# Optimization experiments

Hardware: AMD Instinct MI355X
Metric: run time of the kernel (lower is better)

Reference implementation:

```python
import jax, jax.numpy as jnp
import numpy as np

N, M, T = 8, 4, 500000   # state dim, measurement dim, trajectory length
ITERS = 100


def setup_inputs() -> dict:
    key = jax.random.key(0)
    k1, k2, k3, k4 = jax.random.split(key, 4)
    xs = jax.random.normal(k1, (N, T), dtype=jnp.float32)
    ys = jax.random.normal(k2, (M, T), dtype=jnp.float32)
    # Well-conditioned, stable models: F near identity, modest H, SPD noise covs.
    F = jnp.eye(N, dtype=jnp.float32) + 0.01 * jax.random.normal(k3, (N, N), dtype=jnp.float32)
    H = 0.1 * jax.random.normal(k4, (M, N), dtype=jnp.float32)
    Q = jnp.eye(N, dtype=jnp.float32)
    R = jnp.eye(M, dtype=jnp.float32)
    gamma = jnp.float32(0.01)
    return {"xs": xs, "ys": ys, "F": F, "H": H, "Q": Q, "R": R, "gamma": gamma}


def reference(xs, ys, F, H, Q, R, gamma):
    # Precompute the message operators (done once in __init__ in the original).
    Qinv = jnp.linalg.inv(Q)
    Rinv = jnp.linalg.inv(R)
    negQinv = -Qinv            # n x n
    FtQinv = F.T @ Qinv        # n x n
    HtRinv = H.T @ Rinv        # n x m

    def step(x, _):
        # x: n x T. Shift columns to get x_{t-1} and x_{t+1} (edge-replicated).
        x_past = jnp.concatenate([x[:, :1], x[:, :-1]], axis=1)
        x_fut = jnp.concatenate([x[:, 1:], x[:, -1:]], axis=1)
        # diff_past_curr: x_t - F x_{t-1}, with ROW 0 zeroed (faithful to res[0]=0.0)
        d1 = (x - F @ x_past).at[0].set(0.0)
        # diff_curr_fut: x_{t+1} - F x_t, with LAST ROW zeroed (faithful to res[-1]=0.0)
        d2 = (x_fut - F @ x).at[-1].set(0.0)
        # diff_y_curr: y - H x_t
        d3 = ys - H @ x
        m = negQinv @ d1 + FtQinv @ d2 + HtRinv @ d3
        return x + gamma * m, None

    x, _ = jax.lax.scan(step, xs, None, length=ITERS)
    return x
```

## Files before the change

kernel.cpp:

```cpp
#include <hip/hip_runtime.h>

#define TLEN   500000
#define NITER  100
#define DHALF  6
#define NOFF   (2*DHALF+1)
#define STRIP  20
#define EWIN   32
#define CT     256
#define NCONV  ((TLEN - 2*STRIP + CT - 1) / CT)

__global__ __launch_bounds__(256) void band_and_edges(
    const float* __restrict__ xs, const float* __restrict__ ys,
    const float* __restrict__ F, const float* __restrict__ H,
    const float* __restrict__ Q, const float* __restrict__ R,
    const float* __restrict__ gam,
    float* __restrict__ wout,
    float* __restrict__ out)
{
  __shared__ double dQaug[8][16];
  __shared__ double dRaug[4][8];
  __shared__ double dFtQi[64], dHtRi[32], dA1[64], dB2[64];
  __shared__ float fmats[224];
  __shared__ __align__(16) float st[2][34][8];

  const int tid = threadIdx.x;
  const int b   = blockIdx.x;
  const int r8  = (tid >> 3) & 7;
  const int c8  = tid & 7;

  if (tid < 64) {
    dQaug[r8][c8]     = (double)Q[r8*8 + c8];
    dQaug[r8][c8 + 8] = (c8 == r8) ? 1.0 : 0.0;
  } else if (tid < 96) {
    int t = tid - 64, rr = t >> 3, cr = t & 7;
    dRaug[rr][cr] = (cr < 4) ? (double)R[rr*4 + cr] : ((cr - 4 == rr) ? 1.0 : 0.0);
  }
  __syncthreads();
  for (int col = 0; col < 8; ++col) {
    double piv = 1, fq = 0, p1 = 0, p2 = 0, m1 = 0, m2 = 0;
    double rpiv = 1, frr = 0, pr = 0, mr = 0;
    const bool doQ = tid < 64;
    const bool doR = (tid >= 64 && tid < 96 && col < 4);
    if (doQ) {
      piv = dQaug[col][col]; fq = dQaug[r8][col];
      p1 = dQaug[col][c8];   p2 = dQaug[col][c8 + 8];
      m1 = dQaug[r8][c8];    m2 = dQaug[r8][c8 + 8];
    }
    if (doR) {
      int t = tid - 64, rr = t >> 3, cr = t & 7;
      rpiv = dRaug[col][col]; frr = dRaug[rr][col];
      pr = dRaug[col][cr];    mr = dRaug[rr][cr];
    }
    __syncthreads();
    if (doQ) {
      dQaug[r8][c8]     = (r8 == col) ? m1 / piv : m1 - fq * (p1 / piv);
      dQaug[r8][c8 + 8] = (r8 == col) ? m2 / piv : m2 - fq * (p2 / piv);
    }
    if (doR) {
      int t = tid - 64, rr = t >> 3, cr = t & 7;
      dRaug[rr][cr] = (rr == col) ? mr / rpiv : mr - frr * (pr / rpiv);
    }
    __syncthreads();
  }
  if (tid < 64) {
    double s = 0.0;
    #pragma unroll
    for (int k = 0; k < 8; ++k) s += (double)F[k*8 + r8] * dQaug[k][c8 + 8];
    dFtQi[r8*8 + c8] = s;
    dA1[r8*8 + c8] = (c8 == 0) ? 0.0 : -dQaug[r8][c8 + 8];
  } else if (tid < 96) {
    int t = tid - 64, i = t >> 2, j = t & 3;
    double s = 0.0;
    #pragma unroll
    for (int k = 0; k < 4; ++k) s += (double)H[k*8 + i] * dRaug[k][j + 4];
    dHtRi[i*4 + j] = s;
  }
  __syncthreads();
  if (tid < 64) dB2[r8*8 + c8] = (c8 == 7) ? 0.0 : dFtQi[r8*8 + c8];
  __syncthreads();
  {
    const double g = (double)gam[0];
    if (tid < 64) {
      double sp = 0.0;
      #pragma unroll
      for (int k = 0; k < 8; ++k) sp -= dA1[r8*8 + k] * (double)F[k*8 + c8];
      double t2 = dA1[r8*8 + c8];
      #pragma unroll
      for (int k = 0; k < 8; ++k) t2 -= dB2[r8*8 + k] * (double)F[k*8 + c8];
      #pragma unroll
      for (int k = 0; k < 4; ++k) t2 -= dHtRi[r8*4 + k] * (double)H[k*8 + c8];
      fmats[       c8*8 + r8] = (float)(((r8 == c8) ? 1.0 : 0.0) + g * t2);
      fmats[ 64 +  c8*8 + r8] = (float)(g * sp);
      fmats[128 +  c8*8 + r8] = (float)(g * dB2[r8*8 + c8]);
    } else if (tid < 96) {
      int t = tid - 64, i = t >> 2, j = t & 3;
      fmats[192 + j*8 + i] = (float)(g * dHtRi[i*4 + j]);
    }
  }
  __syncthreads();

  const int i = tid & 7;
  const int g = tid >> 3;
  float cmr[8], pmr[8], fur[7];
  #pragma unroll
  for (int k = 0; k < 8; ++k) {
    cmr[k] = fmats[       k*8 + i];
    pmr[k] = fmats[ 64 +  k*8 + i];
    if (k < 7) fur[k] = fmats[128 + k*8 + i];
  }
  float* const stf = (float*)st;
  const int BUF = 34*8;

  if (b < 12) {
    const int c = b;
    const bool act = tid < NOFF*8;
    const int s = g + 1;
    for (int idx = tid; idx < 2*BUF; idx += 256) stf[idx] = 0.0f;
    __syncthreads();
    if (act && c < 8 && s == DHALF + 1 && i == c) st[0][s][i] = 1.0f;
    const float seed = (act && c >= 8 && s == DHALF + 1) ? fmats[192 + (c - 8)*8 + i] : 0.0f;
    __syncthreads();
    int p = 0;
    float last = 0.0f;
    #pragma unroll 1
    for (int it = 0; it < NITER; ++it) {
      if (act) {
        const float* sp_ = stf + p*BUF;
        const float4 o0 = *(const float4*)(sp_ + s*8);
        const float4 o1 = *(const float4*)(sp_ + s*8 + 4);
        const float4 u0 = *(const float4*)(sp_ + (s + 1)*8);
        const float4 u1 = *(const float4*)(sp_ + (s + 1)*8 + 4);
        const float4 d0 = *(const float4*)(sp_ + (s - 1)*8);
        const float4 d1 = *(const float4*)(sp_ + (s - 1)*8 + 4);
        float a0 = seed, a1 = 0.0f, a2 = 0.0f;
        a0 = fmaf(cmr[0], o0.x, a0); a0 = fmaf(cmr[1], o0.y, a0);
        a0 = fmaf(cmr[2], o0.z, a0); a0 = fmaf(cmr[3], o0.w, a0);
        a0 = fmaf(cmr[4], o1.x, a0); a0 = fmaf(cmr[5], o1.y, a0);
        a0 = fmaf(cmr[6], o1.z, a0); a0 = fmaf(cmr[7], o1.w, a0);
        a1 = fmaf(pmr[0], u0.x, a1); a1 = fmaf(pmr[1], u0.y, a1);
        a1 = fmaf(pmr[2], u0.z, a1); a1 = fmaf(pmr[3], u0.w, a1);
        a1 = fmaf(pmr[4], u1.x, a1); a1 = fmaf(pmr[5], u1.y, a1);
        a1 = fmaf(pmr[6], u1.z, a1); a1 = fmaf(pmr[7], u1.w, a1);
        a2 = fmaf(fur[0], d0.x, a2); a2 = fmaf(fur[1], d0.y, a2);
        a2 = fmaf(fur[2], d0.z, a2); a2 = fmaf(fur[3], d0.w, a2);
        a2 = fmaf(fur[4], d1.x, a2); a2 = fmaf(fur[5], d1.y, a2);
        a2 = fmaf(fur[6], d1.z, a2);
        last = a0 + a1 + a2;
        stf[(p^1)*BUF + s*8 + i] = last;
      }
      __syncthreads();
      p ^= 1;
    }
    if (act) wout[(c*NOFF + (s - 1))*8 + i] = last;
    return;
  }

  const bool left = (b == 12);
  const int col  = g;
  const int gcol = left ? col : (TLEN - EWIN + col);
  const int sL = (col > 0) ? col - 1 : 0;
  const int sR = (col < EWIN - 1) ? col + 1 : EWIN - 1;
  const float xv = xs[i*TLEN + gcol];
  float gyv;
  {
    gyv = fmats[192 +      i] * ys[0*TLEN + gcol];
    gyv = fmaf(fmats[192 +  8 + i], ys[1*TLEN + gcol], gyv);
    gyv = fmaf(fmats[192 + 16 + i], ys[2*TLEN + gcol], gyv);
    gyv = fmaf(fmats[192 + 24 + i], ys[3*TLEN + gcol], gyv);
  }
  st[0][col][i] = xv;
  __syncthreads();
  int p = 0;
  float last = xv;
  #pragma unroll 1
  for (int it = 0; it < NITER; ++it) {
    const float* sp_ = stf + p*BUF;
    const float4 o0 = *(const float4*)(sp_ + col*8);
    const float4 o1 = *(const float4*)(sp_ + col*8 + 4);
    const float4 l0 = *(const float4*)(sp_ + sL*8);
    const float4 l1 = *(const float4*)(sp_ + sL*8 + 4);
    const float4 q0 = *(const float4*)(sp_ + sR*8);
    const float4 q1 = *(const float4*)(sp_ + sR*8 + 4);
    float a0 = gyv, a1 = 0.0f, a2 = 0.0f;
    a0 = fmaf(cmr[0], o0.x, a0); a0 = fmaf(cmr[1], o0.y, a0);
    a0 = fmaf(cmr[2], o0.z, a0); a0 = fmaf(cmr[3], o0.w, a0);
    a0 = fmaf(cmr[4], o1.x, a0); a0 = fmaf(cmr[5], o1.y, a0);
    a0 = fmaf(cmr[6], o1.z, a0); a0 = fmaf(cmr[7], o1.w, a0);
    a1 = fmaf(pmr[0], l0.x, a1); a1 = fmaf(pmr[1], l0.y, a1);
    a1 = fmaf(pmr[2], l0.z, a1); a1 = fmaf(pmr[3], l0.w, a1);
    a1 = fmaf(pmr[4], l1.x, a1); a1 = fmaf(pmr[5], l1.y, a1);
    a1 = fmaf(pmr[6], l1.z, a1); a1 = fmaf(pmr[7], l1.w, a1);
    a2 = fmaf(fur[0], q0.x, a2); a2 = fmaf(fur[1], q0.y, a2);
    a2 = fmaf(fur[2], q0.z, a2); a2 = fmaf(fur[3], q0.w, a2);
    a2 = fmaf(fur[4], q1.x, a2); a2 = fmaf(fur[5], q1.y, a2);
    a2 = fmaf(fur[6], q1.z, a2);
    last = a0 + a1 + a2;
    stf[(p^1)*BUF + col*8 + i] = last;
    __syncthreads();
    p ^= 1;
  }
  if (left ? (col < STRIP) : (col >= EWIN - STRIP)) out[i*TLEN + gcol] = last;
}

__global__ __launch_bounds__(CT) void kgm_conv(
    const float* __restrict__ xs, const float* __restrict__ ys,
    const float* __restrict__ wq, float* __restrict__ out)
{
  const int tid  = threadIdx.x;
  const int ocol = STRIP + blockIdx.x * CT + tid;
  const int col  = (ocol < TLEN - STRIP) ? ocol : (TLEN - STRIP - 1);

  float acc[8] = {0,0,0,0,0,0,0,0};
  #pragma unroll
  for (int k = 0; k < 12; ++k) {
    const float* src = (k < 8) ? (xs + k*TLEN + col) : (ys + (k-8)*TLEN + col);
    const float* wk  = wq + k*(NOFF*8);
    float z[NOFF];
    #pragma unroll
    for (int d = 0; d < NOFF; ++d) z[d] = src[d - DHALF];
    #pragma unroll
    for (int d = 0; d < NOFF; ++d) {
      #pragma unroll
      for (int i = 0; i < 8; ++i)
        acc[i] = fmaf(wk[d*8 + i], z[d], acc[i]);
    }
  }

  if (ocol < TLEN - STRIP) {
    #pragma unroll
    for (int i = 0; i < 8; ++i) out[i*TLEN + ocol] = acc[i];
  }
}

extern "C" void kernel_launch(void* const* d_in, const int* in_sizes, int n_in,
                              void* d_out, int out_size, void* d_ws, size_t ws_size,
                              hipStream_t stream)
{
  (void)in_sizes; (void)n_in; (void)out_size; (void)ws_size;
  const float* xs = (const float*)d_in[0];
  const float* ys = (const float*)d_in[1];
  const float* F  = (const float*)d_in[2];
  const float* H  = (const float*)d_in[3];
  const float* Q  = (const float*)d_in[4];
  const float* R  = (const float*)d_in[5];
  const float* ga = (const float*)d_in[6];
  float* ws  = (float*)d_ws;
  float* out = (float*)d_out;
  band_and_edges<<<14, 256, 0, stream>>>(xs, ys, F, H, Q, R, ga, ws, out);
  kgm_conv<<<NCONV, CT, 0, stream>>>(xs, ys, ws, out);
}
```

Before: 53.23 us.

## Compute two columns per thread in conv kernel with LDS-staged weights

The banded convolution kernel now gives each thread two adjacent output columns. Each input row is read once as float2 loads over a 14-wide window and shared across both outputs, and the per-offset weights are staged into LDS with a padded 128-float row stride and read as float4. The weight workspace layout is changed to that padded stride, with the pad zero-filled by the band kernel. Block size drops to 64 threads and the grid halves. This is meant to cut redundant global loads and weight fetches per FMA, at the cost of more registers and fewer threads in flight.

```diff
diff --git a/kernel.cpp b/kernel.cpp
--- a/kernel.cpp
+++ b/kernel.cpp
@@ -6,8 +6,10 @@
 #define NOFF   (2*DHALF+1)
 #define STRIP  20
 #define EWIN   32
-#define CT     256
-#define NCONV  ((TLEN - 2*STRIP + CT - 1) / CT)
+#define CT     64
+#define CCPT   2
+#define NCONV  ((TLEN - 2*STRIP + CT*CCPT - 1) / (CT*CCPT))
+#define WROW   128
 
 __global__ __launch_bounds__(256) void band_and_edges(
     const float* __restrict__ xs, const float* __restrict__ ys,
@@ -151,7 +153,8 @@
       __syncthreads();
       p ^= 1;
     }
-    if (act) wout[(c*NOFF + (s - 1))*8 + i] = last;
+    if (act) wout[c*WROW + (s - 1)*8 + i] = last;
+    if (tid >= NOFF*8 && tid < WROW) wout[c*WROW + tid] = 0.0f;
     return;
   }
 
@@ -206,29 +209,53 @@
     const float* __restrict__ xs, const float* __restrict__ ys,
     const float* __restrict__ wq, float* __restrict__ out)
 {
-  const int tid  = threadIdx.x;
-  const int ocol = STRIP + blockIdx.x * CT + tid;
-  const int col  = (ocol < TLEN - STRIP) ? ocol : (TLEN - STRIP - 1);
-
-  float acc[8] = {0,0,0,0,0,0,0,0};
+  __shared__ __align__(16) float wl[12 * WROW];
+  const int lane = threadIdx.x;
   #pragma unroll
+  for (int t = 0; t < 6; ++t) {
+    const int idx = lane + t*64;
+    *(float4*)(wl + 4*idx) = *(const float4*)(wq + 4*idx);
+  }
+  __syncthreads();
+
+  const int ocol = STRIP + (blockIdx.x * CT + lane) * CCPT;
+  const int col0 = (ocol <= TLEN - STRIP - CCPT) ? ocol : (TLEN - STRIP - CCPT);
+
+  float2 acc[8];
+  #pragma unroll
+  for (int i = 0; i < 8; ++i) acc[i] = make_float2(0.f, 0.f);
+
+  #pragma unroll 2
   for (int k = 0; k < 12; ++k) {
-    const float* src = (k < 8) ? (xs + k*TLEN + col) : (ys + (k-8)*TLEN + col);
-    const float* wk  = wq + k*(NOFF*8);
-    float z[NOFF];
-    #pragma unroll
-    for (int d = 0; d < NOFF; ++d) z[d] = src[d - DHALF];
+    const float* src = ((k < 8) ? (xs + k*TLEN) : (ys + (k-8)*TLEN)) + col0;
+    float z[14];
+    #pragma unroll
+    for (int h = 0; h < 7; ++h) {
+      float2 v = *(const float2*)(src - 6 + 2*h);
+      z[2*h] = v.x; z[2*h + 1] = v.y;
+    }
+    const float* wk = wl + k*WROW;
     #pragma unroll
     for (int d = 0; d < NOFF; ++d) {
       #pragma unroll
-      for (int i = 0; i < 8; ++i)
-        acc[i] = fmaf(wk[d*8 + i], z[d], acc[i]);
+      for (int j = 0; j < 2; ++j) {
+        const float4 w4 = *(const float4*)(wk + d*8 + 4*j);
+        acc[4*j+0].x = fmaf(w4.x, z[d],     acc[4*j+0].x);
+        acc[4*j+0].y = fmaf(w4.x, z[d + 1], acc[4*j+0].y);
+        acc[4*j+1].x = fmaf(w4.y, z[d],     acc[4*j+1].x);
+        acc[4*j+1].y = fmaf(w4.y, z[d + 1], acc[4*j+1].y);
+        acc[4*j+2].x = fmaf(w4.z, z[d],     acc[4*j+2].x);
+        acc[4*j+2].y = fmaf(w4.z, z[d + 1], acc[4*j+2].y);
+        acc[4*j+3].x = fmaf(w4.w, z[d],     acc[4*j+3].x);
+        acc[4*j+3].y = fmaf(w4.w, z[d + 1], acc[4*j+3].y);
+      }
     }
   }
 
   if (ocol < TLEN - STRIP) {
     #pragma unroll
-    for (int i = 0; i < 8; ++i) out[i*TLEN + ocol] = acc[i];
+    for (int i = 0; i < 8; ++i)
+      *(float2*)(out + i*TLEN + ocol) = acc[i];
   }
 }
 
```

After: 52.06 us. 2.2% less time.

## Restructure band convolution to register-tile 8 columns per thread with split-K halves

Applied to the files above, without the earlier changes.

The convolution kernel now gives each thread 8 consecutive output columns for one output row, loading input strips with float4 reads and holding that row's weights in registers. The 12 input channels are split between two halves of the block, which are combined through shared memory. The band kernel also writes the weights in a transposed, padded layout to support this. The goal is to cut redundant global loads (previously 13 scalar loads per channel per column) and per-FMA weight loads, at the cost of more registers (80 weights plus 24 inputs), a shared-memory reduction, and a barrier.

```diff
diff --git a/kernel.cpp b/kernel.cpp
--- a/kernel.cpp
+++ b/kernel.cpp
@@ -6,8 +6,9 @@
 #define NOFF   (2*DHALF+1)
 #define STRIP  20
 #define EWIN   32
-#define CT     256
-#define NCONV  ((TLEN - 2*STRIP + CT - 1) / CT)
+#define WROW   128
+#define W2OFF  (12*WROW)
+#define NCONV  ((TLEN - 2*STRIP + 63) / 64)
 
 __global__ __launch_bounds__(256) void band_and_edges(
     const float* __restrict__ xs, const float* __restrict__ ys,
@@ -15,6 +16,7 @@
     const float* __restrict__ Q, const float* __restrict__ R,
     const float* __restrict__ gam,
     float* __restrict__ wout,
+    float* __restrict__ wout2,
     float* __restrict__ out)
 {
   __shared__ double dQaug[8][16];
@@ -151,7 +153,13 @@
       __syncthreads();
       p ^= 1;
     }
-    if (act) wout[(c*NOFF + (s - 1))*8 + i] = last;
+    if (act) {
+      wout[c*WROW + (s - 1)*8 + i] = last;
+      const int h2 = (c >= 6) ? 1 : 0;
+      const int kk = c - h2*6;
+      wout2[i*160 + h2*80 + kk*13 + (s - 1)] = last;
+    }
+    if (tid >= NOFF*8 && tid < WROW) wout[c*WROW + tid] = 0.0f;
     return;
   }
 
@@ -202,33 +210,63 @@
   if (left ? (col < STRIP) : (col >= EWIN - STRIP)) out[i*TLEN + gcol] = last;
 }
 
-__global__ __launch_bounds__(CT) void kgm_conv(
+__global__ __launch_bounds__(128) void kgm_conv(
     const float* __restrict__ xs, const float* __restrict__ ys,
-    const float* __restrict__ wq, float* __restrict__ out)
+    const float* __restrict__ w2, float* __restrict__ out)
 {
-  const int tid  = threadIdx.x;
-  const int ocol = STRIP + blockIdx.x * CT + tid;
-  const int col  = (ocol < TLEN - STRIP) ? ocol : (TLEN - STRIP - 1);
+  __shared__ float part[64 * 8];
+  const int tid = threadIdx.x;
+  const int h   = tid >> 6;
+  const int i   = (tid >> 3) & 7;
+  const int g   = tid & 7;
+  int c0 = STRIP + blockIdx.x * 64 + g * 8;
+  const bool str = (c0 < TLEN - STRIP);
+  if (c0 > TLEN - STRIP - 8) c0 = TLEN - STRIP - 8;
+
+  float wf[80];
+  {
+    const float* wb = w2 + i*160 + h*80;
+    #pragma unroll
+    for (int t = 0; t < 20; ++t) {
+      float4 v = *(const float4*)(wb + 4*t);
+      wf[4*t] = v.x; wf[4*t+1] = v.y; wf[4*t+2] = v.z; wf[4*t+3] = v.w;
+    }
+  }
 
   float acc[8] = {0,0,0,0,0,0,0,0};
   #pragma unroll
-  for (int k = 0; k < 12; ++k) {
-    const float* src = (k < 8) ? (xs + k*TLEN + col) : (ys + (k-8)*TLEN + col);
-    const float* wk  = wq + k*(NOFF*8);
-    float z[NOFF];
-    #pragma unroll
-    for (int d = 0; d < NOFF; ++d) z[d] = src[d - DHALF];
+  for (int r = 0; r < 6; ++r) {
+    const int k = h*6 + r;
+    const float* src = ((k < 8) ? (xs + k*TLEN) : (ys + (k-8)*TLEN)) + c0;
+    float z[24];
+    #pragma unroll
+    for (int t = 0; t < 6; ++t) {
+      float4 v = *(const float4*)(src - 8 + 4*t);
+      z[4*t] = v.x; z[4*t+1] = v.y; z[4*t+2] = v.z; z[4*t+3] = v.w;
+    }
     #pragma unroll
     for (int d = 0; d < NOFF; ++d) {
-      #pragma unroll
-      for (int i = 0; i < 8; ++i)
-        acc[i] = fmaf(wk[d*8 + i], z[d], acc[i]);
-    }
-  }
-
-  if (ocol < TLEN - STRIP) {
-    #pragma unroll
-    for (int i = 0; i < 8; ++i) out[i*TLEN + ocol] = acc[i];
+      const float w = wf[r*13 + d];
+      #pragma unroll
+      for (int j = 0; j < 8; ++j)
+        acc[j] = fmaf(w, z[d + 2 + j], acc[j]);
+    }
+  }
+
+  if (h == 1) {
+    #pragma unroll
+    for (int j = 0; j < 8; ++j) part[(i*8 + g)*8 + j] = acc[j];
+  }
+  __syncthreads();
+  if (h == 0 && str) {
+    const float* pp = part + (i*8 + g)*8;
+    float4 o0, o1;
+    o0.x = acc[0] + pp[0]; o0.y = acc[1] + pp[1];
+    o0.z = acc[2] + pp[2]; o0.w = acc[3] + pp[3];
+    o1.x = acc[4] + pp[4]; o1.y = acc[5] + pp[5];
+    o1.z = acc[6] + pp[6]; o1.w = acc[7] + pp[7];
+    *(float4*)(out + i*TLEN + c0)     = o0;
+    *(float4*)(out + i*TLEN + c0 + 4) = o1;
   }
 }
 
@@ -246,6 +284,6 @@
   const float* ga = (const float*)d_in[6];
   float* ws  = (float*)d_ws;
   float* out = (float*)d_out;
-  band_and_edges<<<14, 256, 0, stream>>>(xs, ys, F, H, Q, R, ga, ws, out);
-  kgm_conv<<<NCONV, CT, 0, stream>>>(xs, ys, ws, out);
+  band_and_edges<<<14, 256, 0, stream>>>(xs, ys, F, H, Q, R, ga, ws, ws + W2OFF, out);
+  kgm_conv<<<NCONV, 128, 0, stream>>>(xs, ys, ws + W2OFF, out);
 }
```

After: 68.19 us. 1.28x slower.
